# Kernel tuning notes

Hardware: AMD Instinct MI355X
Metric: run time of the kernel (lower is better)

Reference implementation:

```python
import jax, jax.numpy as jnp
import numpy as np

INPUT_DIM = 512
EMBED_DIM = 64
B, S = 4, 4096


def setup_inputs() -> dict:
    key = jax.random.key(0)
    ks = jax.random.split(key, 9)
    scale = 1.0 / np.sqrt(INPUT_DIM)
    return {
        "q": jax.random.normal(ks[0], (B, S, INPUT_DIM), dtype=jnp.float32),
        "k": jax.random.normal(ks[1], (B, S, INPUT_DIM), dtype=jnp.float32),
        "v": jax.random.normal(ks[2], (B, S, INPUT_DIM), dtype=jnp.float32),
        "Wq": jax.random.uniform(ks[3], (INPUT_DIM, EMBED_DIM), jnp.float32, -scale, scale),
        "bq": jax.random.uniform(ks[4], (EMBED_DIM,), jnp.float32, -scale, scale),
        "Wk": jax.random.uniform(ks[5], (INPUT_DIM, EMBED_DIM), jnp.float32, -scale, scale),
        "bk": jax.random.uniform(ks[6], (EMBED_DIM,), jnp.float32, -scale, scale),
        "Wv": jax.random.uniform(ks[7], (INPUT_DIM, EMBED_DIM), jnp.float32, -scale, scale),
        "bv": jax.random.uniform(ks[8], (EMBED_DIM,), jnp.float32, -scale, scale),
    }


def reference(q, k, v, Wq, bq, Wk, bk, Wv, bv):
    # Linear projections (torch Linear: x @ W^T + b; here W stored as [in, out])
    Q = q @ Wq + bq  # [B, S, E]
    K = k @ Wk + bk  # [B, S, E]
    V = v @ Wv + bv  # [B, S, E]
    d_k = K.shape[-1]
    scores = jnp.einsum("bqe,bke->bqk", Q, K) / jnp.sqrt(jnp.float32(d_k))  # [B, S, S]
    attn = jax.nn.softmax(scores, axis=-1)
    return jnp.einsum("bqk,bke->bqe", attn, V)  # [B, S, E]
```

## Files before the change

kernel.cpp:

```cpp
#include <hip/hip_runtime.h>
#include <math.h>

#define S_ 4096
#define C_SCALE 0.18033688011112042f
#define KSPLIT 8

typedef __attribute__((ext_vector_type(4))) float  floatx4;
typedef __attribute__((ext_vector_type(4))) short  short4_t;
typedef __attribute__((ext_vector_type(8))) short  short8_t;
typedef __attribute__((ext_vector_type(2))) unsigned int uintx2;
typedef __attribute__((ext_vector_type(4))) unsigned int uintx4;

__device__ __forceinline__ short f2bf(float f) {
  unsigned u = __builtin_bit_cast(unsigned, f);
  u += 0x7FFFu + ((u >> 16) & 1u);
  return (short)(u >> 16);
}
__device__ __forceinline__ unsigned pack2(float lo, float hi) {
  unsigned a = __builtin_bit_cast(unsigned, lo) + 0x8000u;
  unsigned b = __builtin_bit_cast(unsigned, hi) + 0x8000u;
  return __builtin_amdgcn_perm(b, a, 0x07060302u);
}
__device__ __forceinline__ void dma16(const void* g, void* l) {
  __builtin_amdgcn_global_load_lds(
      (const __attribute__((address_space(1))) void*)g,
      (__attribute__((address_space(3))) void*)l, 16, 0, 0);
}

__global__ __launch_bounds__(256) void prep_w(const float* __restrict__ Wq,
                                              const float* __restrict__ Wk,
                                              const float* __restrict__ Wv,
                                              short* __restrict__ Wt) {
  __shared__ float T[64 * 65];
  int m = blockIdx.x >> 3, kt = blockIdx.x & 7, tid = threadIdx.x;
  const float* W = (m == 0) ? Wq : (m == 1) ? Wk : Wv;
  float sc = (m == 0) ? C_SCALE : 1.0f;
#pragma unroll
  for (int i = 0; i < 16; i++) {
    int e = i * 256 + tid;
    int k = e >> 6, n = e & 63;
    T[k * 65 + n] = W[(kt * 64 + k) * 64 + n];
  }
  __syncthreads();
#pragma unroll
  for (int i = 0; i < 16; i++) {
    int e = i * 256 + tid;
    int n = e >> 6, k = e & 63;
    Wt[m * 32768 + n * 512 + kt * 64 + k] = f2bf(T[k * 65 + n] * sc);
  }
}

__global__ __launch_bounds__(256, 3) void proj_kernel(
    const float* __restrict__ qin, const float* __restrict__ kin,
    const float* __restrict__ vin, const float* __restrict__ bq,
    const float* __restrict__ bk, const float* __restrict__ bv,
    const short* __restrict__ Wt, short* __restrict__ Qp,
    short* __restrict__ Kp, short* __restrict__ Vt) {
  __shared__ float A_lds[2][64 * 64];
  __shared__ short W_lds[2][64 * 64];

  int tid = threadIdx.x;
  int m = blockIdx.x >> 8;
  int r0 = (blockIdx.x & 255) * 64;
  int wid = tid >> 6, lane = tid & 63, l15 = lane & 15, quad = lane >> 4;
  int key = l15 & 7;

  const float* in = (m == 0) ? qin : (m == 1) ? kin : vin;
  const short* Wm = Wt + m * 32768;

  floatx4 acc[4];
#pragma unroll
  for (int nb = 0; nb < 4; nb++) acc[nb] = (floatx4){0.f, 0.f, 0.f, 0.f};

  auto stage = [&](int kc, int buf) {
#pragma unroll
    for (int j = 0; j < 4; j++) {
      int slot = wid * 256 + j * 64 + lane;
      int r = slot >> 4, c = slot & 15;
      int gc = (c & 8) | ((c ^ r) & 7);
      dma16(in + (size_t)(r0 + r) * 512 + kc * 64 + gc * 4,
            (void*)&A_lds[buf][(wid * 4 + j) * 256]);
    }
#pragma unroll
    for (int j = 0; j < 2; j++) {
      int slot = wid * 128 + j * 64 + lane;
      int r = slot >> 3, c = slot & 7;
      int gc = (c ^ (r & 7)) * 8;
      dma16(Wm + r * 512 + kc * 64 + gc, (void*)&W_lds[buf][(wid * 2 + j) * 512]);
    }
  };

  stage(0, 0);
  for (int kc = 0; kc < 8; kc++) {
    __syncthreads();
    if (kc < 7) stage(kc + 1, (kc + 1) & 1);
    __syncthreads();
    const float* Ab = A_lds[kc & 1];
    const short* Wb = W_lds[kc & 1];
    int arow = wid * 16 + l15;
#pragma unroll
    for (int h = 0; h < 2; h++) {
      floatx4 a0 = *(const floatx4*)(Ab + arow * 64 + ((h * 8) | ((quad * 2) ^ key)) * 4);
      floatx4 a1 = *(const floatx4*)(Ab + arow * 64 + ((h * 8) | ((quad * 2 + 1) ^ key)) * 4);
      uintx4 af = {pack2(a0[0], a0[1]), pack2(a0[2], a0[3]),
                   pack2(a1[0], a1[1]), pack2(a1[2], a1[3])};
      short8_t afv = __builtin_bit_cast(short8_t, af);
#pragma unroll
      for (int nb = 0; nb < 4; nb++) {
        short8_t wf = *(const short8_t*)(Wb + (nb * 16 + l15) * 64 +
                                         (((h * 4 + quad) ^ key)) * 8);
        acc[nb] = __builtin_amdgcn_mfma_f32_16x16x32_bf16(afv, wf, acc[nb], 0, 0, 0);
      }
    }
  }

  const float* bias = (m == 0) ? bq : (m == 1) ? bk : bv;
  float bsc = (m == 0) ? C_SCALE : 1.0f;
  if (m < 2) {
    short* out = (m == 0) ? Qp : Kp;
#pragma unroll
    for (int nb = 0; nb < 4; nb++) {
      float bv_ = bias[nb * 16 + l15] * bsc;
#pragma unroll
      for (int r = 0; r < 4; r++)
        out[(size_t)(r0 + wid * 16 + quad * 4 + r) * 64 + nb * 16 + l15] =
            f2bf(acc[nb][r] + bv_);
    }
  } else {
    int bb = r0 >> 12;
    int s0 = (r0 & 4095) + wid * 16 + quad * 4;
#pragma unroll
    for (int nb = 0; nb < 4; nb++) {
      float bv_ = bias[nb * 16 + l15];
      short4_t pk = {f2bf(acc[nb][0] + bv_), f2bf(acc[nb][1] + bv_),
                     f2bf(acc[nb][2] + bv_), f2bf(acc[nb][3] + bv_)};
      *(short4_t*)(Vt + (size_t)bb * 262144 + (nb * 16 + l15) * 4096 + s0) = pk;
    }
  }
}

__global__ __launch_bounds__(256, 2) void attn_kernel(
    const short* __restrict__ Qp, const short* __restrict__ Kp,
    const short* __restrict__ Vt, float* __restrict__ Po,
    float* __restrict__ Lp) {
  __shared__ short K_lds[2][64 * 64];
  __shared__ short V_lds[2][64 * 64];
  __shared__ short P_lds[4][64 * 64];

  int tid = threadIdx.x;
  int ks = blockIdx.x >> 6, b = (blockIdx.x >> 4) & 3, qt = blockIdx.x & 15;
  int wid = tid >> 6, lane = tid & 63, l15 = lane & 15, quad = lane >> 4;
  int key = l15 & 7;

  const short* Qb = Qp + (size_t)b * (S_ * 64);
  const short* Kb = Kp + (size_t)b * (S_ * 64);
  const short* Vb = Vt + (size_t)b * (64 * S_);

  int q0 = qt * 256 + wid * 64;

  short8_t qf[4][2];
#pragma unroll
  for (int qs = 0; qs < 4; qs++)
#pragma unroll
    for (int h = 0; h < 2; h++)
      qf[qs][h] = *(const short8_t*)(Qb + (q0 + qs * 16 + l15) * 64 + h * 32 + quad * 8);

  floatx4 o[4][4];
#pragma unroll
  for (int qs = 0; qs < 4; qs++)
#pragma unroll
    for (int eb = 0; eb < 4; eb++) o[qs][eb] = (floatx4){0.f, 0.f, 0.f, 0.f};
  float l_acc[4] = {0.f, 0.f, 0.f, 0.f};
  short* Pw = &P_lds[wid][0];
  int ks_base = ks * 512;

  auto stage = [&](int t, int buf) {
    int ks0 = ks_base + t * 64;
#pragma unroll
    for (int j = 0; j < 2; j++) {
      int slot = wid * 128 + j * 64 + lane;
      int r = slot >> 3, c = slot & 7;
      int gc = (c ^ (r & 7)) * 8;
      dma16(Kb + (ks0 + r) * 64 + gc, (void*)&K_lds[buf][(wid * 2 + j) * 512]);
      dma16(Vb + (size_t)r * 4096 + ks0 + gc, (void*)&V_lds[buf][(wid * 2 + j) * 512]);
    }
  };

  stage(0, 0);
  for (int t = 0; t < 8; t++) {
    __syncthreads();
    if (t < 7) stage(t + 1, (t + 1) & 1);
    __syncthreads();
    const short* Kt = K_lds[t & 1];
    const short* Vl = V_lds[t & 1];

#pragma unroll
    for (int jh = 0; jh < 2; jh++) {
      short8_t kA[4];
#pragma unroll
      for (int jb = 0; jb < 2; jb++)
#pragma unroll
        for (int eh = 0; eh < 2; eh++)
          kA[jb * 2 + eh] = *(const short8_t*)(
              Kt + (jh * 32 + jb * 16 + l15) * 64 + ((eh * 4 + quad) ^ key) * 8);

#pragma unroll
      for (int qs = 0; qs < 4; qs++) {
        floatx4 z = (floatx4){0.f, 0.f, 0.f, 0.f};
        floatx4 s0 = __builtin_amdgcn_mfma_f32_16x16x32_bf16(kA[0], qf[qs][0], z, 0, 0, 0);
        s0 = __builtin_amdgcn_mfma_f32_16x16x32_bf16(kA[1], qf[qs][1], s0, 0, 0, 0);
        floatx4 s1 = __builtin_amdgcn_mfma_f32_16x16x32_bf16(kA[2], qf[qs][0], z, 0, 0, 0);
        s1 = __builtin_amdgcn_mfma_f32_16x16x32_bf16(kA[3], qf[qs][1], s1, 0, 0, 0);
        float e00 = __builtin_amdgcn_exp2f(s0[0]), e01 = __builtin_amdgcn_exp2f(s0[1]);
        float e02 = __builtin_amdgcn_exp2f(s0[2]), e03 = __builtin_amdgcn_exp2f(s0[3]);
        float e10 = __builtin_amdgcn_exp2f(s1[0]), e11 = __builtin_amdgcn_exp2f(s1[1]);
        float e12 = __builtin_amdgcn_exp2f(s1[2]), e13 = __builtin_amdgcn_exp2f(s1[3]);
        l_acc[qs] += ((e00 + e01) + (e02 + e03)) + ((e10 + e11) + (e12 + e13));
        int row = (qs * 16 + l15) * 64;
        uintx2 w0 = {pack2(e00, e01), pack2(e02, e03)};
        uintx2 w1 = {pack2(e10, e11), pack2(e12, e13)};
        *(uintx2*)(Pw + row + ((jh * 4 + 0 + (quad >> 1)) ^ key) * 8 + (quad & 1) * 4) = w0;
        *(uintx2*)(Pw + row + ((jh * 4 + 2 + (quad >> 1)) ^ key) * 8 + (quad & 1) * 4) = w1;
      }

      short8_t pf[4];
#pragma unroll
      for (int qs = 0; qs < 4; qs++)
        pf[qs] = *(const short8_t*)(Pw + (qs * 16 + l15) * 64 +
                                    ((jh * 4 + quad) ^ key) * 8);
#pragma unroll
      for (int eb = 0; eb < 4; eb++) {
        short8_t vf = *(const short8_t*)(Vl + (eb * 16 + l15) * 64 +
                                         ((jh * 4 + quad) ^ key) * 8);
#pragma unroll
        for (int qs = 0; qs < 4; qs++)
          o[qs][eb] = __builtin_amdgcn_mfma_f32_16x16x32_bf16(pf[qs], vf, o[qs][eb], 0, 0, 0);
      }
    }
  }

#pragma unroll
  for (int qs = 0; qs < 4; qs++) {
    float l = l_acc[qs];
    l += __shfl_xor(l, 16, 64);
    l += __shfl_xor(l, 32, 64);
    int grow_base = b * 4096 + q0 + qs * 16;
    size_t pb = ((size_t)ks * 16384 + grow_base) * 64;
#pragma unroll
    for (int eb = 0; eb < 4; eb++)
#pragma unroll
      for (int r = 0; r < 4; r++)
        Po[pb + (size_t)(quad * 4 + r) * 64 + eb * 16 + l15] = o[qs][eb][r];
    if (quad == 0) Lp[ks * 16384 + grow_base + l15] = l;
  }
}

__global__ __launch_bounds__(256) void combine_kernel(
    const float* __restrict__ Po, const float* __restrict__ Lp,
    float* __restrict__ out) {
  int gid = blockIdx.x * 256 + threadIdx.x;
  int grow = gid >> 4, e0 = (gid & 15) * 4;
  floatx4 s = (floatx4){0.f, 0.f, 0.f, 0.f};
  float l = 0.f;
#pragma unroll
  for (int ks = 0; ks < KSPLIT; ks++) {
    s += *(const floatx4*)(Po + ((size_t)ks * 16384 + grow) * 64 + e0);
    l += Lp[ks * 16384 + grow];
  }
  *(floatx4*)(out + (size_t)grow * 64 + e0) = s * (1.0f / l);
}

extern "C" void kernel_launch(void* const* d_in, const int* in_sizes, int n_in,
                              void* d_out, int out_size, void* d_ws, size_t ws_size,
                              hipStream_t stream) {
  const float* q = (const float*)d_in[0];
  const float* k = (const float*)d_in[1];
  const float* v = (const float*)d_in[2];
  const float* Wq = (const float*)d_in[3];
  const float* bq = (const float*)d_in[4];
  const float* Wk = (const float*)d_in[5];
  const float* bk = (const float*)d_in[6];
  const float* Wv = (const float*)d_in[7];
  const float* bv = (const float*)d_in[8];

  char* ws = (char*)d_ws;
  short* Qp = (short*)(ws);
  short* Kp = (short*)(ws + (1u << 21));
  short* Vt = (short*)(ws + (2u << 21));
  short* Wt = (short*)(ws + (3u << 21));
  float* Po = (float*)(ws + (4u << 21));
  float* Lp = (float*)(ws + (20u << 21));

  prep_w<<<24, 256, 0, stream>>>(Wq, Wk, Wv, Wt);
  proj_kernel<<<768, 256, 0, stream>>>(q, k, v, bq, bk, bv, Wt, Qp, Kp, Vt);
  attn_kernel<<<512, 256, 0, stream>>>(Qp, Kp, Vt, Po, Lp);
  combine_kernel<<<1024, 256, 0, stream>>>(Po, Lp, (float*)d_out);
}
```

Measured before the change: 172.6 us.

## Stage projection inputs as bf16 in LDS and store split-K partials in bf16

The projection kernel now loads fp32 inputs into registers, converts them to bf16 once, and writes them to a single swizzled bf16 LDS tile. Previously it DMA'd fp32 tiles into double-buffered LDS and converted them on every read. The attention kernel now writes its split-K partial outputs as bf16 instead of fp32, which halves partial-buffer traffic for both the attention store and the combine read. P packing switches to truncation instead of rounding. The bf16 partials and truncated P add accuracy loss, and dropping LDS double buffering for A and W may expose load latency.

```diff
diff --git a/kernel.cpp b/kernel.cpp
--- a/kernel.cpp
+++ b/kernel.cpp
@@ -20,6 +20,13 @@
   unsigned a = __builtin_bit_cast(unsigned, lo) + 0x8000u;
   unsigned b = __builtin_bit_cast(unsigned, hi) + 0x8000u;
   return __builtin_amdgcn_perm(b, a, 0x07060302u);
+}
+__device__ __forceinline__ unsigned packt(float lo, float hi) {
+  return __builtin_amdgcn_perm(__builtin_bit_cast(unsigned, hi),
+                               __builtin_bit_cast(unsigned, lo), 0x07060302u);
+}
+__device__ __forceinline__ float bf2f(short s) {
+  return __builtin_bit_cast(float, (unsigned)((unsigned short)s) << 16);
 }
 __device__ __forceinline__ void dma16(const void* g, void* l) {
   __builtin_amdgcn_global_load_lds(
@@ -56,60 +63,66 @@
     const float* __restrict__ bk, const float* __restrict__ bv,
     const short* __restrict__ Wt, short* __restrict__ Qp,
     short* __restrict__ Kp, short* __restrict__ Vt) {
-  __shared__ float A_lds[2][64 * 64];
-  __shared__ short W_lds[2][64 * 64];
+  __shared__ short A_lds[64 * 64];
+  __shared__ short W_lds[64 * 64];
 
   int tid = threadIdx.x;
   int m = blockIdx.x >> 8;
   int r0 = (blockIdx.x & 255) * 64;
   int wid = tid >> 6, lane = tid & 63, l15 = lane & 15, quad = lane >> 4;
-  int key = l15 & 7;
 
   const float* in = (m == 0) ? qin : (m == 1) ? kin : vin;
   const short* Wm = Wt + m * 32768;
 
-  floatx4 acc[4];
-#pragma unroll
-  for (int nb = 0; nb < 4; nb++) acc[nb] = (floatx4){0.f, 0.f, 0.f, 0.f};
-
-  auto stage = [&](int kc, int buf) {
-#pragma unroll
-    for (int j = 0; j < 4; j++) {
-      int slot = wid * 256 + j * 64 + lane;
-      int r = slot >> 4, c = slot & 15;
-      int gc = (c & 8) | ((c ^ r) & 7);
-      dma16(in + (size_t)(r0 + r) * 512 + kc * 64 + gc * 4,
-            (void*)&A_lds[buf][(wid * 4 + j) * 256]);
-    }
+  int sr = tid >> 3, sc = tid & 7;
+  int sphys = ((sc ^ (sr & 7)) * 8);
+
+  floatx4 ar[4];
+  auto loadA = [&](int kc) {
+    const float* p = in + (size_t)(r0 + sr) * 512 + kc * 64 + sc * 8;
+    ar[0] = *(const floatx4*)p;
+    ar[1] = *(const floatx4*)(p + 4);
+    const float* p2 = p + 32 * 512;
+    ar[2] = *(const floatx4*)p2;
+    ar[3] = *(const floatx4*)(p2 + 4);
+  };
+  auto dmaW = [&](int kc) {
 #pragma unroll
     for (int j = 0; j < 2; j++) {
       int slot = wid * 128 + j * 64 + lane;
       int r = slot >> 3, c = slot & 7;
       int gc = (c ^ (r & 7)) * 8;
-      dma16(Wm + r * 512 + kc * 64 + gc, (void*)&W_lds[buf][(wid * 2 + j) * 512]);
+      dma16(Wm + r * 512 + kc * 64 + gc, (void*)&W_lds[(wid * 2 + j) * 512]);
     }
   };
 
-  stage(0, 0);
+  floatx4 acc[4];
+#pragma unroll
+  for (int nb = 0; nb < 4; nb++) acc[nb] = (floatx4){0.f, 0.f, 0.f, 0.f};
+
+  loadA(0);
+#pragma unroll
   for (int kc = 0; kc < 8; kc++) {
+    if (kc) __syncthreads();
+    dmaW(kc);
+    uintx4 w0 = {pack2(ar[0][0], ar[0][1]), pack2(ar[0][2], ar[0][3]),
+                 pack2(ar[1][0], ar[1][1]), pack2(ar[1][2], ar[1][3])};
+    uintx4 w1 = {pack2(ar[2][0], ar[2][1]), pack2(ar[2][2], ar[2][3]),
+                 pack2(ar[3][0], ar[3][1]), pack2(ar[3][2], ar[3][3])};
+    *(short8_t*)(A_lds + sr * 64 + sphys) = __builtin_bit_cast(short8_t, w0);
+    *(short8_t*)(A_lds + (sr + 32) * 64 + sphys) = __builtin_bit_cast(short8_t, w1);
+    if (kc < 7) loadA(kc + 1);
     __syncthreads();
-    if (kc < 7) stage(kc + 1, (kc + 1) & 1);
-    __syncthreads();
-    const float* Ab = A_lds[kc & 1];
-    const short* Wb = W_lds[kc & 1];
     int arow = wid * 16 + l15;
+    int akey = arow & 7, wkey = l15 & 7;
 #pragma unroll
     for (int h = 0; h < 2; h++) {
-      floatx4 a0 = *(const floatx4*)(Ab + arow * 64 + ((h * 8) | ((quad * 2) ^ key)) * 4);
-      floatx4 a1 = *(const floatx4*)(Ab + arow * 64 + ((h * 8) | ((quad * 2 + 1) ^ key)) * 4);
-      uintx4 af = {pack2(a0[0], a0[1]), pack2(a0[2], a0[3]),
-                   pack2(a1[0], a1[1]), pack2(a1[2], a1[3])};
-      short8_t afv = __builtin_bit_cast(short8_t, af);
+      short8_t af = *(const short8_t*)(A_lds + arow * 64 + ((h * 4 + quad) ^ akey) * 8);
 #pragma unroll
       for (int nb = 0; nb < 4; nb++) {
-        short8_t wf = *(const short8_t*)(Wb + (nb * 16 + l15) * 64 +
-                                         (((h * 4 + quad) ^ key)) * 8);
-        acc[nb] = __builtin_amdgcn_mfma_f32_16x16x32_bf16(afv, wf, acc[nb], 0, 0, 0);
+        short8_t wf = *(const short8_t*)(W_lds + (nb * 16 + l15) * 64 +
+                                         ((h * 4 + quad) ^ wkey) * 8);
+        acc[nb] = __builtin_amdgcn_mfma_f32_16x16x32_bf16(af, wf, acc[nb], 0, 0, 0);
       }
     }
   }
@@ -141,7 +154,7 @@
 
 __global__ __launch_bounds__(256, 2) void attn_kernel(
     const short* __restrict__ Qp, const short* __restrict__ Kp,
-    const short* __restrict__ Vt, float* __restrict__ Po,
+    const short* __restrict__ Vt, short* __restrict__ Po,
     float* __restrict__ Lp) {
   __shared__ short K_lds[2][64 * 64];
   __shared__ short V_lds[2][64 * 64];
@@ -217,8 +230,8 @@
         float e12 = __builtin_amdgcn_exp2f(s1[2]), e13 = __builtin_amdgcn_exp2f(s1[3]);
         l_acc[qs] += ((e00 + e01) + (e02 + e03)) + ((e10 + e11) + (e12 + e13));
         int row = (qs * 16 + l15) * 64;
-        uintx2 w0 = {pack2(e00, e01), pack2(e02, e03)};
-        uintx2 w1 = {pack2(e10, e11), pack2(e12, e13)};
+        uintx2 w0 = {packt(e00, e01), packt(e02, e03)};
+        uintx2 w1 = {packt(e10, e11), packt(e12, e13)};
         *(uintx2*)(Pw + row + ((jh * 4 + 0 + (quad >> 1)) ^ key) * 8 + (quad & 1) * 4) = w0;
         *(uintx2*)(Pw + row + ((jh * 4 + 2 + (quad >> 1)) ^ key) * 8 + (quad & 1) * 4) = w1;
       }
@@ -245,29 +258,37 @@
     l += __shfl_xor(l, 16, 64);
     l += __shfl_xor(l, 32, 64);
     int grow_base = b * 4096 + q0 + qs * 16;
-    size_t pb = ((size_t)ks * 16384 + grow_base) * 64;
+    short* Pb = Po + ((size_t)ks * 16384 + grow_base) * 64;
 #pragma unroll
     for (int eb = 0; eb < 4; eb++)
 #pragma unroll
       for (int r = 0; r < 4; r++)
-        Po[pb + (size_t)(quad * 4 + r) * 64 + eb * 16 + l15] = o[qs][eb][r];
+        Pb[(size_t)(quad * 4 + r) * 64 + eb * 16 + l15] = f2bf(o[qs][eb][r]);
     if (quad == 0) Lp[ks * 16384 + grow_base + l15] = l;
   }
 }
 
 __global__ __launch_bounds__(256) void combine_kernel(
-    const float* __restrict__ Po, const float* __restrict__ Lp,
+    const short* __restrict__ Po, const float* __restrict__ Lp,
     float* __restrict__ out) {
   int gid = blockIdx.x * 256 + threadIdx.x;
-  int grow = gid >> 4, e0 = (gid & 15) * 4;
-  floatx4 s = (floatx4){0.f, 0.f, 0.f, 0.f};
+  int grow = gid >> 3, e0 = (gid & 7) * 8;
+  float s[8];
+#pragma unroll
+  for (int i = 0; i < 8; i++) s[i] = 0.f;
   float l = 0.f;
 #pragma unroll
   for (int ks = 0; ks < KSPLIT; ks++) {
-    s += *(const floatx4*)(Po + ((size_t)ks * 16384 + grow) * 64 + e0);
+    short8_t p = *(const short8_t*)(Po + ((size_t)ks * 16384 + grow) * 64 + e0);
+#pragma unroll
+    for (int i = 0; i < 8; i++) s[i] += bf2f(p[i]);
     l += Lp[ks * 16384 + grow];
   }
-  *(floatx4*)(out + (size_t)grow * 64 + e0) = s * (1.0f / l);
+  float inv = 1.0f / l;
+  floatx4 o0 = {s[0] * inv, s[1] * inv, s[2] * inv, s[3] * inv};
+  floatx4 o1 = {s[4] * inv, s[5] * inv, s[6] * inv, s[7] * inv};
+  *(floatx4*)(out + (size_t)grow * 64 + e0) = o0;
+  *(floatx4*)(out + (size_t)grow * 64 + e0 + 4) = o1;
 }
 
 extern "C" void kernel_launch(void* const* d_in, const int* in_sizes, int n_in,
@@ -288,11 +309,11 @@
   short* Kp = (short*)(ws + (1u << 21));
   short* Vt = (short*)(ws + (2u << 21));
   short* Wt = (short*)(ws + (3u << 21));
-  float* Po = (float*)(ws + (4u << 21));
-  float* Lp = (float*)(ws + (20u << 21));
+  short* Po = (short*)(ws + (4u << 21));
+  float* Lp = (float*)(ws + (13u << 21));
 
   prep_w<<<24, 256, 0, stream>>>(Wq, Wk, Wv, Wt);
   proj_kernel<<<768, 256, 0, stream>>>(q, k, v, bq, bk, bv, Wt, Qp, Kp, Vt);
   attn_kernel<<<512, 256, 0, stream>>>(Qp, Kp, Vt, Po, Lp);
-  combine_kernel<<<1024, 256, 0, stream>>>(Po, Lp, (float*)d_out);
-}
+  combine_kernel<<<512, 256, 0, stream>>>(Po, Lp, (float*)d_out);
+}
```

Result: faster. 165.3 us (-4.2%).
